# Performance work log

Hardware: AMD Instinct MI355X
Metric: run time of the kernel (lower is better)

## Reference

```python
import jax, jax.numpy as jnp
import numpy as np

B, Q, K, DQ, DK, DV, H = 16, 64, 512, 512, 512, 512, 256
MASK_VAL = -1e6


def setup_inputs() -> dict:
    key = jax.random.key(0)
    k1, k2, k3, k4, k5, k6, k7 = jax.random.split(key, 7)
    return {
        "queries": jax.random.normal(k1, (B, Q, DQ), dtype=jnp.float32),
        "keys": jax.random.normal(k2, (B, K, DK), dtype=jnp.float32),
        "values": jax.random.normal(k3, (B, K, DV), dtype=jnp.float32),
        "valid_lens": jax.random.randint(k4, (B,), 1, K + 1, dtype=jnp.int32),
        "Wq": jax.random.normal(k5, (DQ, H), dtype=jnp.float32) * (1.0 / np.sqrt(DQ)),
        "Wk": jax.random.normal(k6, (DK, H), dtype=jnp.float32) * (1.0 / np.sqrt(DK)),
        "Wv": jax.random.normal(k7, (H,), dtype=jnp.float32) * (1.0 / np.sqrt(H)),
    }


def reference(queries, keys, values, valid_lens, Wq, Wk, Wv):
    # Project queries and keys into the shared additive-attention space.
    q = jnp.einsum("bqd,dh->bqh", queries, Wq)   # [B,Q,H]
    k = jnp.einsum("bkd,dh->bkh", keys, Wk)      # [B,K,H]
    # Bahdanau additive scoring: tanh(q + k) projected to a scalar per (q,k).
    feats = jnp.tanh(q[:, :, None, :] + k[:, None, :, :])  # [B,Q,K,H]
    scores = jnp.einsum("bqkh,h->bqk", feats, Wv)           # [B,Q,K]
    # Masked softmax over the key axis (positions >= valid_len masked out).
    mask = jnp.arange(K)[None, None, :] < valid_lens[:, None, None]  # [B,1,K]
    scores = jnp.where(mask, scores, MASK_VAL)
    attn = jax.nn.softmax(scores, axis=-1)                  # [B,Q,K]
    # Dropout is identity in eval mode; weighted sum of values.
    return jnp.einsum("bqk,bkv->bqv", attn, values)         # [B,Q,DV]
```

## Files before the change

### kernel.cpp

```cpp
#include <hip/hip_runtime.h>

#define LOG2E 1.4426950408889634f
#define TWO_LOG2E 2.8853900817779268f

typedef __attribute__((ext_vector_type(8))) short short8;
typedef __attribute__((ext_vector_type(4))) float f32x4;

__device__ __forceinline__ float e2x(float v) {
    return __builtin_amdgcn_exp2f(v * TWO_LOG2E);
}

__device__ __forceinline__ void split2(float x, float y, unsigned& hi, unsigned& lo) {
    unsigned ux = __float_as_uint(x), uy = __float_as_uint(y);
    float hx = __uint_as_float(ux & 0xffff0000u);
    float hy = __uint_as_float(uy & 0xffff0000u);
    unsigned lx = __float_as_uint(x - hx), ly = __float_as_uint(y - hy);
    hi = (ux >> 16) | (uy & 0xffff0000u);
    lo = (lx >> 16) | (ly & 0xffff0000u);
}

__global__ __launch_bounds__(256) void wprep_kernel(const float* __restrict__ Wq,
                                                    const float* __restrict__ Wk,
                                                    ushort* __restrict__ Wq2T,
                                                    ushort* __restrict__ Wk2T) {
    __shared__ float T[64][65];
    const float* W  = blockIdx.z ? Wk : Wq;
    ushort* W2T     = blockIdx.z ? Wk2T : Wq2T;
    const int t  = threadIdx.x;
    const int k0 = blockIdx.x * 64;
    const int n0 = blockIdx.y * 64;
#pragma unroll
    for (int p = 0; p < 4; ++p) {
        int u  = t + p * 256;
        int kk = u >> 4;
        int nf = (u & 15) * 4;
        float4 w = *reinterpret_cast<const float4*>(&W[(size_t)(k0 + kk) * 256 + n0 + nf]);
        T[nf + 0][kk] = w.x; T[nf + 1][kk] = w.y;
        T[nf + 2][kk] = w.z; T[nf + 3][kk] = w.w;
    }
    __syncthreads();
#pragma unroll
    for (int p = 0; p < 4; ++p) {
        int u  = t + p * 256;
        int n  = u >> 4;
        int kf = (u & 15) * 4;
        float a = T[n][kf], b = T[n][kf + 1], c = T[n][kf + 2], d = T[n][kf + 3];
        unsigned h01, l01, h23, l23;
        split2(a, b, h01, l01);
        split2(c, d, h23, l23);
        int kg   = k0 + kf;
        int ng   = n0 + n;
        int tile = ng >> 6;
        int row  = ng & 63;
        int cc   = kg >> 5;
        int kpos = kg & 31;
        ushort* base = W2T + (size_t)(tile * 16 + cc) * 6144
                     + (kpos >> 3) * 512 + row * 8 + (kpos & 7);
        uint2 hi; hi.x = h01; hi.y = h23;
        uint2 lo; lo.x = l01; lo.y = l23;
        *reinterpret_cast<uint2*>(base)        = hi;
        *reinterpret_cast<uint2*>(base + 2048) = hi;
        *reinterpret_cast<uint2*>(base + 4096) = lo;
    }
}

__global__ __launch_bounds__(256) void mfma_proj_kernel(const float* __restrict__ queries,
                                                        const float* __restrict__ keys,
                                                        const ushort* __restrict__ Wq2T,
                                                        const ushort* __restrict__ Wk2T,
                                                        float* __restrict__ Eq,
                                                        float* __restrict__ Ekp) {
    __shared__ float smemf[4736];
    ushort* Ah = reinterpret_cast<ushort*>(smemf);
    ushort* Bl = reinterpret_cast<ushort*>(smemf) + 3328;

    const int t    = threadIdx.x;
    const int mt   = blockIdx.x;
    const int Nb   = blockIdx.y * 64;
    const bool isQ = mt < 32;
    const int mloc = (isQ ? mt : mt - 32) * 32;
    const float4* Asrc4 = reinterpret_cast<const float4*>(isQ ? queries : keys)
                        + (size_t)mloc * 128;
    const ushort* W2T = isQ ? Wq2T : Wk2T;

    const int ln15 = t & 15;
    const int q    = (t >> 4) & 3;
    const int w    = t >> 6;
    const int wn   = w * 16;
    const int am   = t >> 3;
    const int ak   = t & 7;

    const char* gB[3];
#pragma unroll
    for (int i = 0; i < 3; ++i)
        gB[i] = reinterpret_cast<const char*>(W2T) + (size_t)(Nb >> 6) * 196608
              + i * 4096 + t * 16;

    f32x4 acc[2];
    acc[0] = (f32x4)0.0f;
    acc[1] = (f32x4)0.0f;

    float4 ra = Asrc4[(size_t)am * 128 + ak];

    for (int c = 0; c < 16; ++c) {
        __syncthreads();
#pragma unroll
        for (int i = 0; i < 3; ++i) {
            __builtin_amdgcn_global_load_lds(
                reinterpret_cast<const unsigned int*>(gB[i]),
                reinterpret_cast<unsigned int*>(
                    reinterpret_cast<char*>(smemf) + 6656 + i * 4096 + (t >> 6) * 1024),
                16, 0, 0);
            gB[i] += 12288;
        }
        {
            unsigned h01, l01, h23, l23;
            split2(ra.x, ra.y, h01, l01);
            split2(ra.z, ra.w, h23, l23);
            uint2 hi; hi.x = h01; hi.y = h23;
            uint2 lo; lo.x = l01; lo.y = l23;
            ushort* row = Ah + am * 104 + ak * 4;
            *reinterpret_cast<uint2*>(row)      = hi;
            *reinterpret_cast<uint2*>(row + 32) = lo;
            *reinterpret_cast<uint2*>(row + 64) = hi;
        }
        if (c < 15) ra = Asrc4[(size_t)am * 128 + (c + 1) * 8 + ak];
        __syncthreads();
#pragma unroll
        for (int s = 0; s < 3; ++s) {
            short8 af[2], bf;
#pragma unroll
            for (int fm = 0; fm < 2; ++fm)
                af[fm] = *reinterpret_cast<const short8*>(
                    Ah + (fm * 16 + ln15) * 104 + s * 32 + q * 8);
            bf = *reinterpret_cast<const short8*>(
                Bl + (s * 4 + q) * 512 + (wn + ln15) * 8);
#pragma unroll
            for (int fm = 0; fm < 2; ++fm)
                acc[fm] = __builtin_amdgcn_mfma_f32_16x16x32_bf16(
                    af[fm], bf, acc[fm], 0, 0, 0);
        }
    }

    if (isQ) {
#pragma unroll
        for (int fm = 0; fm < 2; ++fm)
#pragma unroll
            for (int r = 0; r < 4; ++r) {
                int row = mloc + fm * 16 + q * 4 + r;
                int col = Nb + wn + ln15;
                Eq[(size_t)row * 256 + col] = e2x(acc[fm][r]);
            }
    } else {
        __syncthreads();
        float (*Cs)[33] = reinterpret_cast<float(*)[33]>(smemf);
#pragma unroll
        for (int fm = 0; fm < 2; ++fm)
#pragma unroll
            for (int r = 0; r < 4; ++r) {
                int m_l = fm * 16 + q * 4 + r;
                int n_l = wn + ln15;
                Cs[n_l][m_l] = acc[fm][r];
            }
        __syncthreads();
        const int b      = mloc >> 9;
        const int k0h    = (mloc & 511) >> 1;
        const int h2base = Nb >> 1;
        float4* out4 = reinterpret_cast<float4*>(Ekp);
#pragma unroll
        for (int p = 0; p < 2; ++p) {
            int u   = t + p * 256;
            int h2r = u >> 4;
            int kp  = u & 15;
            int kk  = kp * 2;
            float4 o;
            o.x = e2x(Cs[2 * h2r    ][kk    ]);
            o.y = e2x(Cs[2 * h2r + 1][kk    ]);
            o.z = e2x(Cs[2 * h2r    ][kk + 1]);
            o.w = e2x(Cs[2 * h2r + 1][kk + 1]);
            out4[(size_t)b * 32768 + (size_t)(h2base + h2r) * 256 + k0h + kp] = o;
        }
    }
}

__global__ __launch_bounds__(512) void attn_kernel(
        const float* __restrict__ Eq, const float* __restrict__ Ekp,
        const float* __restrict__ Wv, const int* __restrict__ valid_lens,
        const float* __restrict__ values, float* __restrict__ out) {
    __shared__ __align__(16) float Eqs[4][256];
    __shared__ float Wvs[256];
    __shared__ __align__(16) float P[4][512];
    __shared__ float Sd[8][4];
    __shared__ __align__(16) float2 Pc[4][256];

    const int t   = threadIdx.x;
    const int lid = blockIdx.x;
    const int r  = lid & 7;
    const int j  = lid >> 3;
    const int b  = r + 8 * (j & 1);
    const int q0 = (j >> 1) * 4;

    if (t < 256) {
        const float4* eq4 = reinterpret_cast<const float4*>(Eq + (size_t)(b * 64 + q0) * 256);
        *reinterpret_cast<float4*>(&Eqs[t >> 6][(t & 63) * 4]) = eq4[t];
        Wvs[t] = Wv[t];
    }
    __syncthreads();

    const float2* ekp2 = reinterpret_cast<const float2*>(Ekp) + (size_t)b * 65536 + t;
    float acc[4] = {0.f, 0.f, 0.f, 0.f};
#pragma unroll 8
    for (int h2 = 0; h2 < 128; ++h2) {
        float2 ek = ekp2[h2 * 512];
        float2 wv = *reinterpret_cast<const float2*>(&Wvs[2 * h2]);
#pragma unroll
        for (int q = 0; q < 4; ++q) {
            float2 e = *reinterpret_cast<const float2*>(&Eqs[q][2 * h2]);
            float a0 = fmaf(e.x, ek.x, 1.0f);
            float a1 = fmaf(e.y, ek.y, 1.0f);
            acc[q] = fmaf(fmaf(wv.y, a0, wv.x * a1),
                          __builtin_amdgcn_rcpf(a0 * a1), acc[q]);
        }
    }

    const int vl = valid_lens[b];
    float E[4], part[4];
#pragma unroll
    for (int q = 0; q < 4; ++q) {
        float s = -2.0f * acc[q];
        E[q] = (t < vl) ? __builtin_amdgcn_exp2f(s * LOG2E) : 0.0f;
        part[q] = E[q];
    }
#pragma unroll
    for (int off = 32; off > 0; off >>= 1)
#pragma unroll
        for (int q = 0; q < 4; ++q) part[q] += __shfl_xor(part[q], off);
    if ((t & 63) == 0) {
#pragma unroll
        for (int q = 0; q < 4; ++q) Sd[t >> 6][q] = part[q];
    }
    __syncthreads();
#pragma unroll
    for (int q = 0; q < 4; ++q) {
        float d = ((Sd[0][q] + Sd[1][q]) + (Sd[2][q] + Sd[3][q]))
                + ((Sd[4][q] + Sd[5][q]) + (Sd[6][q] + Sd[7][q]));
        P[q][t] = E[q] * (1.0f / d);
    }
    __syncthreads();

    const int v2c = t & 255;
    const int kh  = t >> 8;
    const float2* V2 = reinterpret_cast<const float2*>(values)
                     + (size_t)b * 131072 + (size_t)(kh * 256) * 256 + v2c;
    float2 av[4];
#pragma unroll
    for (int q = 0; q < 4; ++q) av[q] = make_float2(0.f, 0.f);

#pragma unroll 4
    for (int k4 = 0; k4 < 64; ++k4) {
        float2 v0 = V2[(size_t)(k4 * 4 + 0) * 256];
        float2 v1 = V2[(size_t)(k4 * 4 + 1) * 256];
        float2 v2 = V2[(size_t)(k4 * 4 + 2) * 256];
        float2 v3 = V2[(size_t)(k4 * 4 + 3) * 256];
#pragma unroll
        for (int q = 0; q < 4; ++q) {
            float4 p = *reinterpret_cast<const float4*>(&P[q][kh * 256 + k4 * 4]);
            av[q].x = fmaf(p.x, v0.x, av[q].x); av[q].y = fmaf(p.x, v0.y, av[q].y);
            av[q].x = fmaf(p.y, v1.x, av[q].x); av[q].y = fmaf(p.y, v1.y, av[q].y);
            av[q].x = fmaf(p.z, v2.x, av[q].x); av[q].y = fmaf(p.z, v2.y, av[q].y);
            av[q].x = fmaf(p.w, v3.x, av[q].x); av[q].y = fmaf(p.w, v3.y, av[q].y);
        }
    }

    if (kh == 1) {
#pragma unroll
        for (int q = 0; q < 4; ++q) Pc[q][v2c] = av[q];
    }
    __syncthreads();
    if (kh == 0) {
        float* ob = out + (size_t)(b * 64 + q0) * 512 + 2 * v2c;
#pragma unroll
        for (int q = 0; q < 4; ++q) {
            float2 o = Pc[q][v2c];
            o.x += av[q].x; o.y += av[q].y;
            *reinterpret_cast<float2*>(ob + (size_t)q * 512) = o;
        }
    }
}

extern "C" void kernel_launch(void* const* d_in, const int* in_sizes, int n_in,
                              void* d_out, int out_size, void* d_ws, size_t ws_size,
                              hipStream_t stream) {
    (void)in_sizes; (void)n_in; (void)out_size; (void)ws_size;
    const float* queries    = (const float*)d_in[0];
    const float* keys       = (const float*)d_in[1];
    const float* values     = (const float*)d_in[2];
    const int*   valid_lens = (const int*)d_in[3];
    const float* Wq         = (const float*)d_in[4];
    const float* Wk         = (const float*)d_in[5];
    const float* Wv         = (const float*)d_in[6];
    float* out = (float*)d_out;

    float* ws     = (float*)d_ws;
    float* Eq     = ws;
    float* Ekp    = ws + 262144;
    ushort* Wq2T  = (ushort*)(ws + 2883584);
    ushort* Wk2T  = Wq2T + 393216;

    hipLaunchKernelGGL(wprep_kernel, dim3(8, 4, 2), dim3(256), 0, stream,
                       Wq, Wk, Wq2T, Wk2T);
    hipLaunchKernelGGL(mfma_proj_kernel, dim3(288, 4), dim3(256), 0, stream,
                       queries, keys, Wq2T, Wk2T, Eq, Ekp);
    hipLaunchKernelGGL(attn_kernel, dim3(256), dim3(512), 0, stream,
                       Eq, Ekp, Wv, valid_lens, values, out);
}
```

Baseline: 147.0 us.

## Double attn_kernel threads by splitting H and K reductions across thread halves

The attention kernel goes from 512 to 1024 threads per block. The score loop now splits the hidden dimension in two halves, with partials combined through shared memory. The PV product splits the key range four ways, with a shared-memory reduction at the end. The aim is more parallelism and latency hiding on a grid of only 256 blocks, at the cost of extra LDS traffic, extra barriers and possible register-pressure limits at 1024 threads.

```diff
diff --git a/kernel.cpp b/kernel.cpp
--- a/kernel.cpp
+++ b/kernel.cpp
@@ -183,15 +183,15 @@
     }
 }
 
-__global__ __launch_bounds__(512) void attn_kernel(
+__global__ __launch_bounds__(1024) void attn_kernel(
         const float* __restrict__ Eq, const float* __restrict__ Ekp,
         const float* __restrict__ Wv, const int* __restrict__ valid_lens,
         const float* __restrict__ values, float* __restrict__ out) {
     __shared__ __align__(16) float Eqs[4][256];
     __shared__ float Wvs[256];
     __shared__ __align__(16) float P[4][512];
-    __shared__ float Sd[8][4];
-    __shared__ __align__(16) float2 Pc[4][256];
+    __shared__ float Sd[16][2];
+    __shared__ __align__(16) float Ubuf[6144];
 
     const int t   = threadIdx.x;
     const int lid = blockIdx.x;
@@ -207,64 +207,74 @@
     }
     __syncthreads();
 
-    const float2* ekp2 = reinterpret_cast<const float2*>(Ekp) + (size_t)b * 65536 + t;
+    const int k  = t & 511;
+    const int hh = t >> 9;
+    const float2* ekp2 = reinterpret_cast<const float2*>(Ekp)
+                       + (size_t)b * 65536 + (size_t)(hh * 64) * 512 + k;
     float acc[4] = {0.f, 0.f, 0.f, 0.f};
 #pragma unroll 8
-    for (int h2 = 0; h2 < 128; ++h2) {
-        float2 ek = ekp2[h2 * 512];
-        float2 wv = *reinterpret_cast<const float2*>(&Wvs[2 * h2]);
+    for (int i = 0; i < 64; ++i) {
+        float2 ek = ekp2[i * 512];
+        float2 wv = *reinterpret_cast<const float2*>(&Wvs[hh * 128 + 2 * i]);
 #pragma unroll
         for (int q = 0; q < 4; ++q) {
-            float2 e = *reinterpret_cast<const float2*>(&Eqs[q][2 * h2]);
+            float2 e = *reinterpret_cast<const float2*>(&Eqs[q][hh * 128 + 2 * i]);
             float a0 = fmaf(e.x, ek.x, 1.0f);
             float a1 = fmaf(e.y, ek.y, 1.0f);
             acc[q] = fmaf(fmaf(wv.y, a0, wv.x * a1),
                           __builtin_amdgcn_rcpf(a0 * a1), acc[q]);
         }
     }
+#pragma unroll
+    for (int q = 0; q < 4; ++q) Ubuf[hh * 2048 + q * 512 + k] = acc[q];
+    __syncthreads();
 
     const int vl = valid_lens[b];
-    float E[4], part[4];
-#pragma unroll
-    for (int q = 0; q < 4; ++q) {
-        float s = -2.0f * acc[q];
-        E[q] = (t < vl) ? __builtin_amdgcn_exp2f(s * LOG2E) : 0.0f;
-        part[q] = E[q];
+    const int qb = hh * 2;
+    float E[2], part[2];
+#pragma unroll
+    for (int qq = 0; qq < 2; ++qq) {
+        int q = qb + qq;
+        float s = -2.0f * (Ubuf[q * 512 + k] + Ubuf[2048 + q * 512 + k]);
+        E[qq] = (k < vl) ? __builtin_amdgcn_exp2f(s * LOG2E) : 0.0f;
+        part[qq] = E[qq];
     }
 #pragma unroll
     for (int off = 32; off > 0; off >>= 1)
 #pragma unroll
-        for (int q = 0; q < 4; ++q) part[q] += __shfl_xor(part[q], off);
+        for (int qq = 0; qq < 2; ++qq) part[qq] += __shfl_xor(part[qq], off);
     if ((t & 63) == 0) {
-#pragma unroll
-        for (int q = 0; q < 4; ++q) Sd[t >> 6][q] = part[q];
-    }
-    __syncthreads();
-#pragma unroll
-    for (int q = 0; q < 4; ++q) {
-        float d = ((Sd[0][q] + Sd[1][q]) + (Sd[2][q] + Sd[3][q]))
-                + ((Sd[4][q] + Sd[5][q]) + (Sd[6][q] + Sd[7][q]));
-        P[q][t] = E[q] * (1.0f / d);
+        int wave = t >> 6;
+        Sd[wave][0] = part[0]; Sd[wave][1] = part[1];
+    }
+    __syncthreads();
+#pragma unroll
+    for (int qq = 0; qq < 2; ++qq) {
+        int base = hh * 8;
+        float d = ((Sd[base + 0][qq] + Sd[base + 1][qq]) + (Sd[base + 2][qq] + Sd[base + 3][qq]))
+                + ((Sd[base + 4][qq] + Sd[base + 5][qq]) + (Sd[base + 6][qq] + Sd[base + 7][qq]));
+        P[qb + qq][k] = E[qq] * (1.0f / d);
     }
     __syncthreads();
 
     const int v2c = t & 255;
-    const int kh  = t >> 8;
+    const int kq  = t >> 8;
+    const int k0c = kq * 128;
     const float2* V2 = reinterpret_cast<const float2*>(values)
-                     + (size_t)b * 131072 + (size_t)(kh * 256) * 256 + v2c;
+                     + (size_t)b * 131072 + (size_t)k0c * 256 + v2c;
     float2 av[4];
 #pragma unroll
     for (int q = 0; q < 4; ++q) av[q] = make_float2(0.f, 0.f);
 
 #pragma unroll 4
-    for (int k4 = 0; k4 < 64; ++k4) {
+    for (int k4 = 0; k4 < 32; ++k4) {
         float2 v0 = V2[(size_t)(k4 * 4 + 0) * 256];
         float2 v1 = V2[(size_t)(k4 * 4 + 1) * 256];
         float2 v2 = V2[(size_t)(k4 * 4 + 2) * 256];
         float2 v3 = V2[(size_t)(k4 * 4 + 3) * 256];
 #pragma unroll
         for (int q = 0; q < 4; ++q) {
-            float4 p = *reinterpret_cast<const float4*>(&P[q][kh * 256 + k4 * 4]);
+            float4 p = *reinterpret_cast<const float4*>(&P[q][k0c + k4 * 4]);
             av[q].x = fmaf(p.x, v0.x, av[q].x); av[q].y = fmaf(p.x, v0.y, av[q].y);
             av[q].x = fmaf(p.y, v1.x, av[q].x); av[q].y = fmaf(p.y, v1.y, av[q].y);
             av[q].x = fmaf(p.z, v2.x, av[q].x); av[q].y = fmaf(p.z, v2.y, av[q].y);
@@ -272,17 +282,22 @@
         }
     }
 
-    if (kh == 1) {
-#pragma unroll
-        for (int q = 0; q < 4; ++q) Pc[q][v2c] = av[q];
-    }
-    __syncthreads();
-    if (kh == 0) {
+    float2* Pc = reinterpret_cast<float2*>(Ubuf);
+    if (kq > 0) {
+#pragma unroll
+        for (int q = 0; q < 4; ++q) Pc[((kq - 1) * 4 + q) * 256 + v2c] = av[q];
+    }
+    __syncthreads();
+    if (kq == 0) {
         float* ob = out + (size_t)(b * 64 + q0) * 512 + 2 * v2c;
 #pragma unroll
         for (int q = 0; q < 4; ++q) {
-            float2 o = Pc[q][v2c];
-            o.x += av[q].x; o.y += av[q].y;
+            float2 p1 = Pc[(0 * 4 + q) * 256 + v2c];
+            float2 p2 = Pc[(1 * 4 + q) * 256 + v2c];
+            float2 p3 = Pc[(2 * 4 + q) * 256 + v2c];
+            float2 o;
+            o.x = (av[q].x + p1.x) + (p2.x + p3.x);
+            o.y = (av[q].y + p1.y) + (p2.y + p3.y);
             *reinterpret_cast<float2*>(ob + (size_t)q * 512) = o;
         }
     }
@@ -311,6 +326,6 @@
                        Wq, Wk, Wq2T, Wk2T);
     hipLaunchKernelGGL(mfma_proj_kernel, dim3(288, 4), dim3(256), 0, stream,
                        queries, keys, Wq2T, Wk2T, Eq, Ekp);
-    hipLaunchKernelGGL(attn_kernel, dim3(256), dim3(512), 0, stream,
+    hipLaunchKernelGGL(attn_kernel, dim3(256), dim3(1024), 0, stream,
                        Eq, Ekp, Wv, valid_lens, values, out);
 }
```

Result: faster. 140.7 us (-4.3%).
